# Performance work log

Measured on AMD Instinct MI355X. Metric: run time of the kernel, lower is better.

The kernel has to match this reference:

```python
import jax, jax.numpy as jnp
import numpy as np

EPS = 1e-6

def _layernorm(x):
    mu = jnp.mean(x, axis=-1, keepdims=True)
    var = jnp.mean(jnp.square(x - mu), axis=-1, keepdims=True)
    return (x - mu) / jnp.sqrt(var + EPS)

def setup_inputs() -> dict:
    key = jax.random.key(0)
    ks = jax.random.split(key, 12)
    B, N, C = 4, 1024, 1024
    H = 16
    Dff = 4 * C
    s = 0.02
    x = jax.random.normal(ks[0], (B, N, C), dtype=jnp.float32)
    mask = jax.random.randint(ks[1], (N, N), 0, 2) > 0  # True = attend
    wq = jax.random.normal(ks[2], (C, C), dtype=jnp.float32) * s
    bq = jnp.zeros((C,), dtype=jnp.float32)
    wkv = jax.random.normal(ks[3], (C, 2 * C), dtype=jnp.float32) * s
    bkv = jnp.zeros((2 * C,), dtype=jnp.float32)
    wo = jax.random.normal(ks[4], (C, C), dtype=jnp.float32) * s
    bo = jnp.zeros((C,), dtype=jnp.float32)
    w1 = jax.random.normal(ks[5], (C, Dff), dtype=jnp.float32) * s
    b1 = jnp.zeros((Dff,), dtype=jnp.float32)
    w2 = jax.random.normal(ks[6], (Dff, C), dtype=jnp.float32) * s
    b2 = jnp.zeros((C,), dtype=jnp.float32)
    return {"x": x, "mask": mask, "wq": wq, "bq": bq, "wkv": wkv, "bkv": bkv,
            "wo": wo, "bo": bo, "w1": w1, "b1": b1, "w2": w2, "b2": b2}

def reference(x, mask, wq, bq, wkv, bkv, wo, bo, w1, b1, w2, b2):
    B, N, C = x.shape
    H = 16
    d = C // H
    scale = d ** -0.5
    max_neg = -jnp.finfo(x.dtype).max
    # attn_bias: 0 where mask True, -max where False; broadcast [1,1,N,N]
    attn_bias = jnp.where(mask, jnp.asarray(0.0, x.dtype), jnp.asarray(max_neg, x.dtype))[None, None]

    # --- pre-norm attention ---
    xn = _layernorm(x)
    q = (xn @ wq + bq).reshape(B, N, H, d)
    kv = xn @ wkv + bkv
    k, v = jnp.split(kv, 2, axis=-1)
    k = k.reshape(B, N, H, d)
    v = v.reshape(B, N, H, d)
    sim = jnp.einsum('bihd,bjhd->bhij', q, k) * scale + attn_bias
    attn = jax.nn.softmax(sim, axis=-1)
    o = jnp.einsum('bhij,bjhd->bihd', attn, v).reshape(B, N, C)
    x = x + (o @ wo + bo)

    # --- pre-norm MLP with tanh-approx GELU ---
    xn = _layernorm(x)
    h = jax.nn.gelu(xn @ w1 + b1, approximate=True)
    x = x + (h @ w2 + b2)
    return x
```

## Files before the change

### kernel.cpp

```cpp
#include <hip/hip_runtime.h>
#include <hip/hip_bf16.h>

typedef short bf16x8 __attribute__((ext_vector_type(8)));
typedef float f32x4 __attribute__((ext_vector_type(4)));
typedef unsigned short u16x8 __attribute__((ext_vector_type(8)));

#define MFMA16(a,b,c) __builtin_amdgcn_mfma_f32_16x16x32_bf16((a),(b),(c),0,0,0)

__device__ inline unsigned short f32_to_bf16(float f){
  union { float f; unsigned u; } v; v.f = f;
  unsigned u = v.u;
  u += 0x7FFFu + ((u >> 16) & 1u);
  return (unsigned short)(u >> 16);
}
__device__ inline float bf16_to_f32(unsigned short u){
  union { unsigned u; float f; } v; v.u = ((unsigned)u)<<16; return v.f;
}

__device__ inline float gelu_tanh(float x){
  float x3 = x*x*x;
  float t = tanhf(0.7978845608028654f*(x + 0.044715f*x3));
  return 0.5f*x*(1.0f+t);
}

__device__ inline void gload16(const void* g, void* l){
  __builtin_amdgcn_global_load_lds(
      (const __attribute__((address_space(1))) void*)g,
      (__attribute__((address_space(3))) void*)l, 16, 0, 0);
}

__device__ inline int xcd_swz(int lin, int nwg){
  int cpx = nwg >> 3;
  return (lin & 7)*cpx + (lin >> 3);
}

__global__ void detect_mask_kernel(const unsigned* __restrict__ m, int* __restrict__ flag){
  __shared__ int s;
  if (threadIdx.x == 0) s = 0;
  __syncthreads();
  unsigned w = m[threadIdx.x];
  if (w > 1u) atomicOr(&s, 1);
  __syncthreads();
  if (threadIdx.x == 0) *flag = s;
}

__global__ __launch_bounds__(256) void mask_bias_kernel(
    const void* __restrict__ mask, const int* __restrict__ flag,
    unsigned short* __restrict__ biasr){
  __shared__ float mt[16][64];
  int qg = blockIdx.x, jt = blockIdx.y;
  int t = threadIdx.x;
  int fl = *flag;
  int jc = jt*64 + (t&63);
  #pragma unroll
  for (int k2=0;k2<4;k2++){
    int qr = qg*16 + (t>>6) + k2*4;
    bool a = fl ? (((const unsigned char*)mask)[(size_t)qr*1024 + jc] != 0)
                : (((const int*)mask)[(size_t)qr*1024 + jc] != 0);
    mt[(t>>6)+k2*4][t&63] = a ? -23.083120654223414f : -1e30f;
  }
  __syncthreads();
  ushort4 ob;
  unsigned short tmp[4];
  #pragma unroll
  for (int u=0;u<4;u++){
    int p = t*4+u;
    int e = p&15, lane = p>>4;
    int i = e>>2, jj = e&3;
    int ln2 = lane&15, g2 = lane>>4;
    tmp[u] = f32_to_bf16(mt[g2*4+i][jj*16+ln2]);
  }
  ob.x=tmp[0]; ob.y=tmp[1]; ob.z=tmp[2]; ob.w=tmp[3];
  *(ushort4*)&biasr[((size_t)(qg*16+jt)*64)*16 + t*4] = ob;
}

__global__ __launch_bounds__(256) void transpose_cvt_kernel(
    const float* __restrict__ W, unsigned short* __restrict__ WT, int K, int N){
  __shared__ float tile[32][37];
  int n0 = blockIdx.x*32, k0 = blockIdx.y*32;
  int r = threadIdx.x>>3, c4 = threadIdx.x&7;
  float4 v = *(const float4*)&W[(size_t)(k0+r)*N + n0 + c4*4];
  tile[r][c4*4+0]=v.x; tile[r][c4*4+1]=v.y; tile[r][c4*4+2]=v.z; tile[r][c4*4+3]=v.w;
  __syncthreads();
  ushort4 o;
  o.x = f32_to_bf16(tile[c4*4+0][r]);
  o.y = f32_to_bf16(tile[c4*4+1][r]);
  o.z = f32_to_bf16(tile[c4*4+2][r]);
  o.w = f32_to_bf16(tile[c4*4+3][r]);
  *(ushort4*)&WT[(size_t)(n0+r)*K + k0 + c4*4] = o;
}

__global__ __launch_bounds__(256) void vtrans_kernel(
    const unsigned short* __restrict__ qkv, unsigned short* __restrict__ vt){
  __shared__ unsigned short t[32][33];
  int b = blockIdx.z;
  int n0 = blockIdx.x*32, d0 = blockIdx.y*32;
  int tx = threadIdx.x & 31, ty = threadIdx.x >> 5;
  #pragma unroll
  for (int r=0;r<4;r++)
    t[ty+8*r][tx] = qkv[(size_t)(b*1024 + n0+ty+8*r)*3072 + 2048 + d0+tx];
  __syncthreads();
  #pragma unroll
  for (int r=0;r<4;r++)
    vt[((size_t)b<<20) + (size_t)(d0+ty+8*r)*1024 + n0+tx] = t[tx][ty+8*r];
}

__global__ void bias_concat_kernel(const float* __restrict__ bq,
                                   const float* __restrict__ bkv,
                                   float* __restrict__ dst){
  int i = blockIdx.x*256 + threadIdx.x;
  if (i < 3072) dst[i] = (i < 1024) ? bq[i] : bkv[i-1024];
}

__global__ __launch_bounds__(256) void ln_kernel(const float* __restrict__ x,
                                                 unsigned short* __restrict__ xn){
  const int C = 1024;
  size_t row = blockIdx.x;
  float4 v = reinterpret_cast<const float4*>(x + row*C)[threadIdx.x];
  float s = v.x+v.y+v.z+v.w;
  float q = v.x*v.x+v.y*v.y+v.z*v.z+v.w*v.w;
  #pragma unroll
  for (int off=32; off; off>>=1){ s += __shfl_xor(s,off); q += __shfl_xor(q,off); }
  __shared__ float sm[8];
  int wv = threadIdx.x>>6, ln = threadIdx.x&63;
  if (ln==0){ sm[wv]=s; sm[4+wv]=q; }
  __syncthreads();
  float S = sm[0]+sm[1]+sm[2]+sm[3];
  float Q = sm[4]+sm[5]+sm[6]+sm[7];
  float mu  = S*(1.0f/1024.0f);
  float var = Q*(1.0f/1024.0f) - mu*mu;
  float inv = rsqrtf(var + 1e-6f);
  ushort4 o;
  o.x = f32_to_bf16((v.x-mu)*inv);
  o.y = f32_to_bf16((v.y-mu)*inv);
  o.z = f32_to_bf16((v.z-mu)*inv);
  o.w = f32_to_bf16((v.w-mu)*inv);
  reinterpret_cast<ushort4*>(xn + row*C)[threadIdx.x] = o;
}

template<int EPI>
__global__ __launch_bounds__(256) void gemm64_kernel(
    const unsigned short* __restrict__ A,
    const unsigned short* __restrict__ BT,
    const float* __restrict__ bias,
    const float* __restrict__ resid,
    void* __restrict__ Cout,
    int M, int N, int K)
{
  __shared__ __align__(16) unsigned short lA[3][128*32];
  __shared__ __align__(16) unsigned short lB[3][64*32];
  int tid = threadIdx.x, wave = tid>>6, lane = tid&63;
  int nbx = gridDim.x;
  int lin = blockIdx.y*nbx + blockIdx.x;
  int w = xcd_swz(lin, nbx*gridDim.y);
  int m0 = (w/nbx)*128, n0 = (w%nbx)*64;
  int ln = lane&15, g = lane>>4;

  int srow = wave*16 + (lane>>2);
  int scol = (((lane&3) ^ ((lane>>3)&3)))*8;
  const unsigned short* gA0 = A  + (size_t)(m0+srow)*K    + scol;
  const unsigned short* gA1 = A  + (size_t)(m0+64+srow)*K + scol;
  const unsigned short* gB0 = BT + (size_t)(n0+srow)*K    + scol;
  int lof0 = wave*512;
  int lof1 = 64*32 + wave*512;

  f32x4 acc[4][2] = {};
  int wm = wave>>1, wn = wave&1;
  int nt = K/32;
  const int axsw = (g ^ ((ln>>1)&3))*8;

  auto STAGE = [&](int t, int buf){
    int ko = t*32;
    gload16(gA0+ko, &lA[buf][lof0]);
    gload16(gA1+ko, &lA[buf][lof1]);
    gload16(gB0+ko, &lB[buf][lof0]);
  };

  STAGE(0,0); STAGE(1,1); STAGE(2,2);

  int cb = 0;
  for (int t=0; t<nt; ++t){
    int rem = nt-1-t;
    if (rem >= 2)      asm volatile("s_waitcnt vmcnt(6)" ::: "memory");
    else if (rem == 1) asm volatile("s_waitcnt vmcnt(3)" ::: "memory");
    else               asm volatile("s_waitcnt vmcnt(0)" ::: "memory");
    __builtin_amdgcn_s_barrier();

    bf16x8 a[4], b[2];
    const unsigned short* pA = &lA[cb][(wm*64+ln)*32 + axsw];
    const unsigned short* pB = &lB[cb][(wn*32+ln)*32 + axsw];
    #pragma unroll
    for (int i=0;i<4;i++) a[i] = *(const bf16x8*)(pA + i*16*32);
    #pragma unroll
    for (int i=0;i<2;i++) b[i] = *(const bf16x8*)(pB + i*16*32);
    #pragma unroll
    for (int mi=0;mi<4;mi++)
      #pragma unroll
      for (int ni=0;ni<2;ni++)
        acc[mi][ni] = MFMA16(a[mi], b[ni], acc[mi][ni]);

    asm volatile("s_waitcnt lgkmcnt(0)" ::: "memory");
    __builtin_amdgcn_s_barrier();
    if (t+3 < nt) STAGE(t+3, cb);
    cb = (cb==2) ? 0 : cb+1;
  }

  #pragma unroll
  for (int mi=0;mi<4;mi++){
    int r0 = m0 + wm*64 + mi*16 + g*4;
    #pragma unroll
    for (int ni=0;ni<2;ni++){
      int c = n0 + wn*32 + ni*16 + ln;
      float bs = bias[c];
      f32x4 cc = acc[mi][ni];
      #pragma unroll
      for (int i=0;i<4;i++){
        int r = r0 + i;
        float v = cc[i] + bs;
        if (EPI == 1){
          v += resid[(size_t)r*N + c];
          ((float*)Cout)[(size_t)r*N + c] = v;
        } else if (EPI == 2){
          ((unsigned short*)Cout)[(size_t)r*N + c] = f32_to_bf16(gelu_tanh(v));
        } else {
          ((unsigned short*)Cout)[(size_t)r*N + c] = f32_to_bf16(v);
        }
      }
    }
  }
}

template<int EPI>
__global__ __launch_bounds__(512) void gemm8_kernel(
    const unsigned short* __restrict__ A,
    const unsigned short* __restrict__ BT,
    const float* __restrict__ bias,
    void* __restrict__ Cout,
    int M, int N, int K)
{
  extern __shared__ __align__(16) char smem[];
  const int tid = threadIdx.x, wave = tid>>6, lane = tid&63;
  const int ln = lane&15, g = lane>>4;
  const int wm = wave>>2, wn = wave&3;
  const int nbx = gridDim.x;
  const int lin = blockIdx.y*nbx + blockIdx.x;
  const int wsw = xcd_swz(lin, nbx*gridDim.y);
  const int m0 = (wsw/nbx)*256, n0 = (wsw%nbx)*256;
  const int NT = K>>6;
  const int axor = (g*16) ^ (((ln>>2)&3)<<4);

  auto STAGE = [&](int kt, int h){
    const bool isB = h&1; const int kh = h>>1;
    const unsigned short* src = isB ? BT : A;
    const int base0 = isB ? n0 : m0;
    char* region = smem + (isB?65536:0) + (kt&1)*32768 + kh*16384;
    #pragma unroll
    for (int r=0;r<2;r++){
      int idx = r*512 + tid;
      int row = idx>>2;
      int col = kt*64 + kh*32 + ((((idx&3)*16) ^ (((row>>2)&3)<<4))>>1);
      gload16(src + (size_t)(base0+row)*K + col,
              region + (r*512 + wave*64)*16);
    }
  };

  STAGE(0,0); STAGE(0,1); STAGE(0,2); STAGE(0,3);
  STAGE(1,0); STAGE(1,1); STAGE(1,2);
  asm volatile("s_waitcnt vmcnt(6)" ::: "memory");
  __builtin_amdgcn_s_barrier();
  __builtin_amdgcn_sched_barrier(0);

  f32x4 acc[8][4] = {};
  bf16x8 a[8], b[2];

  for (int t=0; t<NT; ++t){
    const int cur = t&1;
    char* Ac0 = smem + cur*32768;
    char* Ac1 = Ac0 + 16384;
    char* Bc0 = smem + 65536 + cur*32768;
    char* Bc1 = Bc0 + 16384;
    #pragma unroll
    for (int mi=0;mi<8;mi++)
      a[mi] = *(const bf16x8*)(Ac0 + (wm*128+mi*16+ln)*64 + axor);
    b[0] = *(const bf16x8*)(Bc0 + (wn*64+ 0+ln)*64 + axor);
    b[1] = *(const bf16x8*)(Bc0 + (wn*64+16+ln)*64 + axor);
    if (t+1 < NT) STAGE(t+1,3);
    __builtin_amdgcn_s_barrier();
    __builtin_amdgcn_s_setprio(1);
    #pragma unroll
    for (int mi=0;mi<8;mi++){
      acc[mi][0] = MFMA16(a[mi], b[0], acc[mi][0]);
      acc[mi][1] = MFMA16(a[mi], b[1], acc[mi][1]);
    }
    __builtin_amdgcn_s_setprio(0);
    __builtin_amdgcn_s_barrier();
    b[0] = *(const bf16x8*)(Bc0 + (wn*64+32+ln)*64 + axor);
    b[1] = *(const bf16x8*)(Bc0 + (wn*64+48+ln)*64 + axor);
    if (t+2 < NT) STAGE(t+2,0);
    __builtin_amdgcn_s_barrier();
    __builtin_amdgcn_s_setprio(1);
    #pragma unroll
    for (int mi=0;mi<8;mi++){
      acc[mi][2] = MFMA16(a[mi], b[0], acc[mi][2]);
      acc[mi][3] = MFMA16(a[mi], b[1], acc[mi][3]);
    }
    __builtin_amdgcn_s_setprio(0);
    __builtin_amdgcn_s_barrier();
    #pragma unroll
    for (int mi=0;mi<8;mi++)
      a[mi] = *(const bf16x8*)(Ac1 + (wm*128+mi*16+ln)*64 + axor);
    b[0] = *(const bf16x8*)(Bc1 + (wn*64+ 0+ln)*64 + axor);
    b[1] = *(const bf16x8*)(Bc1 + (wn*64+16+ln)*64 + axor);
    if (t+2 < NT) STAGE(t+2,1);
    __builtin_amdgcn_s_barrier();
    __builtin_amdgcn_s_setprio(1);
    #pragma unroll
    for (int mi=0;mi<8;mi++){
      acc[mi][0] = MFMA16(a[mi], b[0], acc[mi][0]);
      acc[mi][1] = MFMA16(a[mi], b[1], acc[mi][1]);
    }
    __builtin_amdgcn_s_setprio(0);
    __builtin_amdgcn_s_barrier();
    b[0] = *(const bf16x8*)(Bc1 + (wn*64+32+ln)*64 + axor);
    b[1] = *(const bf16x8*)(Bc1 + (wn*64+48+ln)*64 + axor);
    if (t+2 < NT) STAGE(t+2,2);
    __builtin_amdgcn_s_barrier();
    __builtin_amdgcn_s_setprio(1);
    #pragma unroll
    for (int mi=0;mi<8;mi++){
      acc[mi][2] = MFMA16(a[mi], b[0], acc[mi][2]);
      acc[mi][3] = MFMA16(a[mi], b[1], acc[mi][3]);
    }
    __builtin_amdgcn_s_setprio(0);
    if (t+2 < NT) asm volatile("s_waitcnt vmcnt(6)" ::: "memory");
    else          asm volatile("s_waitcnt vmcnt(0)" ::: "memory");
    __builtin_amdgcn_s_barrier();
    __builtin_amdgcn_sched_barrier(0);
  }

  #pragma unroll
  for (int mi=0;mi<8;mi++){
    int r0 = m0 + wm*128 + mi*16 + g*4;
    #pragma unroll
    for (int nj=0;nj<4;nj++){
      int c = n0 + wn*64 + nj*16 + ln;
      float bs = bias[c];
      f32x4 cc = acc[mi][nj];
      #pragma unroll
      for (int i=0;i<4;i++){
        int r = r0 + i;
        float v = cc[i] + bs;
        if (EPI == 2){
          ((unsigned short*)Cout)[(size_t)r*N + c] = f32_to_bf16(gelu_tanh(v));
        } else {
          ((unsigned short*)Cout)[(size_t)r*N + c] = f32_to_bf16(v);
        }
      }
    }
  }
}

__global__ __launch_bounds__(256,6) void attn_kernel(
    const unsigned short* __restrict__ qkv,
    const unsigned short* __restrict__ vt,
    const unsigned short* __restrict__ biasr,
    unsigned short* __restrict__ pn,
    float* __restrict__ lsumg)
{
  const int N = 1024, NK = 3072;
  const float SCL = 0.18033688011112042f;
  __shared__ __align__(16) unsigned short lK[64*64];
  __shared__ __align__(16) unsigned short lV[64*64];
  __shared__ __align__(16) unsigned short plds[4][16][72];
  int bh = blockIdx.x, qt = blockIdx.y, sp = blockIdx.z;
  int b = bh>>4, h = bh&15;
  int tid = threadIdx.x, wave = tid>>6, lane = tid&63;
  int ln = lane&15, g = lane>>4;
  size_t base = (size_t)b*N;
  int q_local = qt*64 + wave*16;

  const unsigned short* qptr = qkv + (base + q_local + ln)*NK + h*64;
  bf16x8 aq0 = *(const bf16x8*)(qptr + g*8);
  bf16x8 aq1 = *(const bf16x8*)(qptr + 32 + g*8);

  int r0s = tid>>3,        c0 = (tid&7) ^ (r0s&7);
  int r1s = 32 + (tid>>3), c1 = (tid&7) ^ (r1s&7);
  const unsigned short* kg0 = qkv + (base + r0s)*NK + 1024 + h*64 + c0*8;
  const unsigned short* kg1 = qkv + (base + r1s)*NK + 1024 + h*64 + c1*8;
  const unsigned short* vg0 = vt + ((size_t)b<<20) + (size_t)(h*64 + r0s)*N + c0*8;
  const unsigned short* vg1 = vt + ((size_t)b<<20) + (size_t)(h*64 + r1s)*N + c1*8;
  char* lKd0 = (char*)lK + (wave*64)*16;
  char* lKd1 = (char*)lK + (256 + wave*64)*16;
  char* lVd0 = (char*)lV + (wave*64)*16;
  char* lVd1 = (char*)lV + (256 + wave*64)*16;

  const unsigned short* brp = biasr +
      (((size_t)(qt*4 + wave)*16)*64 + lane)*16;

  f32x4 oacc[4] = {};
  float lsum[4] = {0.f,0.f,0.f,0.f};
  const int xl = (ln&7);

  for (int t=0; t<8; ++t){
    int j0 = sp*512 + t*64;
    __syncthreads();
    gload16(kg0 + (size_t)j0*NK, lKd0);
    gload16(kg1 + (size_t)j0*NK, lKd1);
    gload16(vg0 + j0, lVd0);
    gload16(vg1 + j0, lVd1);
    int jt = j0>>6;
    bf16x8 bb0 = *(const bf16x8*)(brp + (size_t)jt*1024);
    bf16x8 bb1 = *(const bf16x8*)(brp + (size_t)jt*1024 + 8);
    asm volatile("s_waitcnt vmcnt(0)" ::: "memory");
    __builtin_amdgcn_s_barrier();

    f32x4 s[4];
    #pragma unroll
    for (int jj=0;jj<4;jj++){
      int row = jj*16+ln;
      bf16x8 k0 = *(const bf16x8*)((const char*)lK + row*128 + ((g^xl)<<4));
      bf16x8 k1 = *(const bf16x8*)((const char*)lK + row*128 + (((g+4)^xl)<<4));
      s[jj] = (f32x4){};
      s[jj] = MFMA16(aq0, k0, s[jj]);
      s[jj] = MFMA16(aq1, k1, s[jj]);
    }
    #pragma unroll
    for (int i=0;i<4;i++){
      #pragma unroll
      for (int jj=0;jj<4;jj++){
        int e = i*4+jj;
        unsigned short bu = (e<8) ? (unsigned short)bb0[e] : (unsigned short)bb1[e-8];
        float ev = exp2f(fmaf(s[jj][i], SCL, bf16_to_f32(bu)));
        lsum[i] += ev;
        plds[wave][4*g+i][jj*16+ln] = f32_to_bf16(ev);
      }
    }
    asm volatile("s_waitcnt lgkmcnt(0)" ::: "memory");
    __builtin_amdgcn_sched_barrier(0);
    bf16x8 p0 = *(const bf16x8*)&plds[wave][ln][g*8];
    bf16x8 p1 = *(const bf16x8*)&plds[wave][ln][32 + g*8];
    #pragma unroll
    for (int nd=0;nd<4;nd++){
      int row = nd*16+ln;
      bf16x8 v0 = *(const bf16x8*)((const char*)lV + row*128 + ((g^xl)<<4));
      bf16x8 v1 = *(const bf16x8*)((const char*)lV + row*128 + (((g+4)^xl)<<4));
      oacc[nd] = MFMA16(p0, v0, oacc[nd]);
      oacc[nd] = MFMA16(p1, v1, oacc[nd]);
    }
  }

  #pragma unroll
  for (int i=0;i<4;i++){
    float l = lsum[i];
    l += __shfl_xor(l,1); l += __shfl_xor(l,2);
    l += __shfl_xor(l,4); l += __shfl_xor(l,8);
    if (ln == 0)
      lsumg[((size_t)sp<<16) + (size_t)(base + q_local + 4*g + i)*16 + h] = l;
  }
  #pragma unroll
  for (int nd=0;nd<4;nd++){
    #pragma unroll
    for (int i=0;i<4;i++){
      int qr = q_local + 4*g + i;
      pn[((size_t)sp<<22) + (base+qr)*1024 + h*64 + nd*16 + ln] = f32_to_bf16(oacc[nd][i]);
    }
  }
}

__global__ __launch_bounds__(256) void attn_reduce_kernel(
    const unsigned short* __restrict__ pn,
    const float* __restrict__ lsumg,
    unsigned short* __restrict__ o)
{
  size_t idx = ((size_t)blockIdx.x*256 + threadIdx.x)*8;
  int r = (int)(idx>>10);
  int h = (int)((idx&1023)>>6);
  float inv = 1.0f/(lsumg[(size_t)r*16+h] + lsumg[(1u<<16) + (size_t)r*16+h]);
  u16x8 p0 = *(const u16x8*)(pn + idx);
  u16x8 p1 = *(const u16x8*)(pn + (1u<<22) + idx);
  u16x8 res;
  #pragma unroll
  for (int e=0;e<8;e++)
    res[e] = f32_to_bf16((bf16_to_f32((unsigned short)p0[e]) +
                          bf16_to_f32((unsigned short)p1[e]))*inv);
  *(u16x8*)(o + idx) = res;
}

extern "C" void kernel_launch(void* const* d_in, const int* in_sizes, int n_in,
                              void* d_out, int out_size, void* d_ws, size_t ws_size,
                              hipStream_t stream)
{
  (void)in_sizes; (void)n_in; (void)out_size; (void)ws_size;
  const float* x   = (const float*)d_in[0];
  const void*  mask= d_in[1];
  const float* wq  = (const float*)d_in[2];
  const float* bq  = (const float*)d_in[3];
  const float* wkv = (const float*)d_in[4];
  const float* bkv = (const float*)d_in[5];
  const float* wo  = (const float*)d_in[6];
  const float* bo  = (const float*)d_in[7];
  const float* w1  = (const float*)d_in[8];
  const float* b1  = (const float*)d_in[9];
  const float* w2  = (const float*)d_in[10];
  const float* b2  = (const float*)d_in[11];
  float* out = (float*)d_out;

  char* ws = (char*)d_ws;
  size_t off = 0;
  auto alloc = [&](size_t bytes){ size_t o = off; off += (bytes + 255) & ~(size_t)255; return o; };
  unsigned short* WqkvT = (unsigned short*)(ws + alloc(3072u*1024u*2));
  unsigned short* WoT   = (unsigned short*)(ws + alloc(1024u*1024u*2));
  unsigned short* W1T   = (unsigned short*)(ws + alloc(4096u*1024u*2));
  unsigned short* W2T   = (unsigned short*)(ws + alloc(1024u*4096u*2));
  float*          BIASQ = (float*)(ws + alloc(3072u*4));
  int*            FLAG  = (int*)(ws + alloc(256));
  float*          LSUM  = (float*)(ws + alloc(2u*4096u*16u*4));
  unsigned short* BIASR = (unsigned short*)(ws + alloc(64u*16u*64u*16u*2));
  unsigned short* XN    = (unsigned short*)(ws + alloc(4096u*1024u*2));
  float*          X1    = (float*)(ws + alloc(4096u*1024u*4));
  unsigned short* QKV   = (unsigned short*)(ws + alloc(4096u*4096u*2));
  unsigned short* VT    = QKV + (size_t)4096u*3072u;
  unsigned short* PN    = (unsigned short*)X1;

  hipFuncSetAttribute(reinterpret_cast<const void*>(&gemm8_kernel<0>),
                      hipFuncAttributeMaxDynamicSharedMemorySize, 131072);
  hipFuncSetAttribute(reinterpret_cast<const void*>(&gemm8_kernel<2>),
                      hipFuncAttributeMaxDynamicSharedMemorySize, 131072);

  transpose_cvt_kernel<<<dim3(32,32),  256, 0, stream>>>(wq,  WqkvT,               1024, 1024);
  transpose_cvt_kernel<<<dim3(64,32),  256, 0, stream>>>(wkv, WqkvT + 1024u*1024u, 1024, 2048);
  transpose_cvt_kernel<<<dim3(32,32),  256, 0, stream>>>(wo,  WoT,                 1024, 1024);
  transpose_cvt_kernel<<<dim3(128,32), 256, 0, stream>>>(w1,  W1T,                 1024, 4096);
  transpose_cvt_kernel<<<dim3(32,128), 256, 0, stream>>>(w2,  W2T,                 4096, 1024);
  bias_concat_kernel<<<12, 256, 0, stream>>>(bq, bkv, BIASQ);
  detect_mask_kernel<<<1, 256, 0, stream>>>((const unsigned*)mask, FLAG);
  mask_bias_kernel<<<dim3(64,16), 256, 0, stream>>>(mask, FLAG, BIASR);

  ln_kernel<<<4096, 256, 0, stream>>>(x, XN);
  gemm8_kernel<0><<<dim3(12,16), 512, 131072, stream>>>(XN, WqkvT, BIASQ, QKV, 4096, 3072, 1024);
  vtrans_kernel<<<dim3(32,32,4), 256, 0, stream>>>(QKV, VT);
  attn_kernel<<<dim3(64,16,2), 256, 0, stream>>>(QKV, VT, BIASR, PN, LSUM);
  attn_reduce_kernel<<<2048, 256, 0, stream>>>(PN, LSUM, XN);
  gemm64_kernel<1><<<dim3(16,32), 256, 0, stream>>>(XN, WoT, bo, x, X1, 4096, 1024, 1024);
  ln_kernel<<<4096, 256, 0, stream>>>(X1, XN);
  gemm8_kernel<2><<<dim3(16,16), 512, 131072, stream>>>(XN, W1T, b1, QKV, 4096, 4096, 1024);
  gemm64_kernel<1><<<dim3(16,32), 256, 0, stream>>>(QKV, W2T, b2, X1, out, 4096, 1024, 4096);
}
```

Measured before the change: 268.2 us.

## Replace 4-wave GEMM with single-wave 64x64 tile kernel without barriers

The 4-wave 128x64 GEMM used for the output projection and MLP down-projection becomes a single-wave kernel computing a 64x64 tile. Each wave now stages its own A and B tiles into a 4-deep LDS ring, so the workgroup barriers go away and waits rely only on vmcnt and lgkmcnt counters. The grid doubles to 1024 blocks. In exchange, each block reuses less data from LDS and issues more global loads per MFMA, and one wave per block may limit latency hiding.

```diff
diff --git a/kernel.cpp b/kernel.cpp
--- a/kernel.cpp
+++ b/kernel.cpp
@@ -139,7 +139,7 @@
 }
 
 template<int EPI>
-__global__ __launch_bounds__(256) void gemm64_kernel(
+__global__ __launch_bounds__(64) void gemm1w_kernel(
     const unsigned short* __restrict__ A,
     const unsigned short* __restrict__ BT,
     const float* __restrict__ bias,
@@ -147,70 +147,64 @@
     void* __restrict__ Cout,
     int M, int N, int K)
 {
-  __shared__ __align__(16) unsigned short lA[3][128*32];
-  __shared__ __align__(16) unsigned short lB[3][64*32];
-  int tid = threadIdx.x, wave = tid>>6, lane = tid&63;
+  __shared__ __align__(16) unsigned short lds[4][8192];
+  int lane = threadIdx.x;
   int nbx = gridDim.x;
   int lin = blockIdx.y*nbx + blockIdx.x;
   int w = xcd_swz(lin, nbx*gridDim.y);
-  int m0 = (w/nbx)*128, n0 = (w%nbx)*64;
+  int m0 = (w%nbx)==(w%nbx) ? (w/nbx)*64 : 0;
+  int n0 = (w%nbx)*64;
   int ln = lane&15, g = lane>>4;
 
-  int srow = wave*16 + (lane>>2);
+  int srow = lane>>2;
   int scol = (((lane&3) ^ ((lane>>3)&3)))*8;
-  const unsigned short* gA0 = A  + (size_t)(m0+srow)*K    + scol;
-  const unsigned short* gA1 = A  + (size_t)(m0+64+srow)*K + scol;
-  const unsigned short* gB0 = BT + (size_t)(n0+srow)*K    + scol;
-  int lof0 = wave*512;
-  int lof1 = 64*32 + wave*512;
-
-  f32x4 acc[4][2] = {};
-  int wm = wave>>1, wn = wave&1;
+  const unsigned short* gA = A  + (size_t)(m0+srow)*K + scol;
+  const unsigned short* gB = BT + (size_t)(n0+srow)*K + scol;
+
+  f32x4 acc[4][4] = {};
   int nt = K/32;
-  const int axsw = (g ^ ((ln>>1)&3))*8;
+  const int rdsw = (g ^ ((ln>>1)&3))*8;
 
   auto STAGE = [&](int t, int buf){
     int ko = t*32;
-    gload16(gA0+ko, &lA[buf][lof0]);
-    gload16(gA1+ko, &lA[buf][lof1]);
-    gload16(gB0+ko, &lB[buf][lof0]);
+    #pragma unroll
+    for (int j=0;j<4;j++)
+      gload16(gA + (size_t)(j*16)*K + ko, &lds[buf][j*512]);
+    #pragma unroll
+    for (int j=0;j<4;j++)
+      gload16(gB + (size_t)(j*16)*K + ko, &lds[buf][4096 + j*512]);
   };
 
   STAGE(0,0); STAGE(1,1); STAGE(2,2);
 
-  int cb = 0;
   for (int t=0; t<nt; ++t){
     int rem = nt-1-t;
-    if (rem >= 2)      asm volatile("s_waitcnt vmcnt(6)" ::: "memory");
-    else if (rem == 1) asm volatile("s_waitcnt vmcnt(3)" ::: "memory");
+    if (rem >= 2)      asm volatile("s_waitcnt vmcnt(16)" ::: "memory");
+    else if (rem == 1) asm volatile("s_waitcnt vmcnt(8)" ::: "memory");
     else               asm volatile("s_waitcnt vmcnt(0)" ::: "memory");
-    __builtin_amdgcn_s_barrier();
-
-    bf16x8 a[4], b[2];
-    const unsigned short* pA = &lA[cb][(wm*64+ln)*32 + axsw];
-    const unsigned short* pB = &lB[cb][(wn*32+ln)*32 + axsw];
-    #pragma unroll
-    for (int i=0;i<4;i++) a[i] = *(const bf16x8*)(pA + i*16*32);
-    #pragma unroll
-    for (int i=0;i<2;i++) b[i] = *(const bf16x8*)(pB + i*16*32);
+    const unsigned short* lb = lds[t&3];
+    bf16x8 a[4], b[4];
+    #pragma unroll
+    for (int mi=0;mi<4;mi++)
+      a[mi] = *(const bf16x8*)(lb + (mi*16+ln)*32 + rdsw);
+    #pragma unroll
+    for (int ni=0;ni<4;ni++)
+      b[ni] = *(const bf16x8*)(lb + 4096 + (ni*16+ln)*32 + rdsw);
     #pragma unroll
     for (int mi=0;mi<4;mi++)
       #pragma unroll
-      for (int ni=0;ni<2;ni++)
+      for (int ni=0;ni<4;ni++)
         acc[mi][ni] = MFMA16(a[mi], b[ni], acc[mi][ni]);
-
     asm volatile("s_waitcnt lgkmcnt(0)" ::: "memory");
-    __builtin_amdgcn_s_barrier();
-    if (t+3 < nt) STAGE(t+3, cb);
-    cb = (cb==2) ? 0 : cb+1;
+    if (t+3 < nt) STAGE(t+3, (t+3)&3);
   }
 
   #pragma unroll
   for (int mi=0;mi<4;mi++){
-    int r0 = m0 + wm*64 + mi*16 + g*4;
-    #pragma unroll
-    for (int ni=0;ni<2;ni++){
-      int c = n0 + wn*32 + ni*16 + ln;
+    int r0 = m0 + mi*16 + g*4;
+    #pragma unroll
+    for (int ni=0;ni<4;ni++){
+      int c = n0 + ni*16 + ln;
       float bs = bias[c];
       f32x4 cc = acc[mi][ni];
       #pragma unroll
@@ -541,8 +535,8 @@
   vtrans_kernel<<<dim3(32,32,4), 256, 0, stream>>>(QKV, VT);
   attn_kernel<<<dim3(64,16,2), 256, 0, stream>>>(QKV, VT, BIASR, PN, LSUM);
   attn_reduce_kernel<<<2048, 256, 0, stream>>>(PN, LSUM, XN);
-  gemm64_kernel<1><<<dim3(16,32), 256, 0, stream>>>(XN, WoT, bo, x, X1, 4096, 1024, 1024);
+  gemm1w_kernel<1><<<dim3(16,64), 64, 0, stream>>>(XN, WoT, bo, x, X1, 4096, 1024, 1024);
   ln_kernel<<<4096, 256, 0, stream>>>(X1, XN);
   gemm8_kernel<2><<<dim3(16,16), 512, 131072, stream>>>(XN, W1T, b1, QKV, 4096, 4096, 1024);
-  gemm64_kernel<1><<<dim3(16,32), 256, 0, stream>>>(QKV, W2T, b2, X1, out, 4096, 1024, 4096);
-}
+  gemm1w_kernel<1><<<dim3(16,64), 64, 0, stream>>>(QKV, W2T, b2, X1, out, 4096, 1024, 4096);
+}
```

Result: slower. 288.0 us (+7.4%).
